# Kernel tuning notes

Hardware: AMD Instinct MI355X
Metric: run time of the kernel (lower is better)

## Reference

```python
import jax, jax.numpy as jnp
import numpy as np

INP = 256
OUP = 256
FGROUP = 16
CGROUP = 8
K = 3
STRIDE = 1
PAD = K // 2
B, H, W = 16, 64, 64
O1 = OUP * INP * K * K // CGROUP  # 73728, glgf output channels


def setup_inputs() -> dict:
    key = jax.random.key(0)
    ks = jax.random.split(key, 11)
    s = 0.1  # keep sigmoid pre-activations in a sane range
    return {
        "x": jax.random.normal(ks[0], (B, INP, H, W), jnp.float32),
        # GLGF generating the dynamic conv weights (oup*inp*k*k//cgroup outputs)
        "g1_fc1_l": jax.random.normal(ks[1], (INP, INP // FGROUP), jnp.float32) * s,
        "g1_fc1_g1": jax.random.normal(ks[2], (FGROUP, INP // FGROUP), jnp.float32) * s,
        "g1_fc1_g2": jax.random.normal(ks[3], (INP, FGROUP), jnp.float32) * s,
        "g1_fc2_l": jax.random.normal(ks[4], (O1,), jnp.float32) * s,
        "g1_fc2_g": jax.random.normal(ks[5], (INP,), jnp.float32) * s,
        # GLGF generating the per-channel output gate c (oup outputs)
        "g2_fc1_l": jax.random.normal(ks[6], (INP, INP // FGROUP), jnp.float32) * s,
        "g2_fc1_g1": jax.random.normal(ks[7], (FGROUP, INP // FGROUP), jnp.float32) * s,
        "g2_fc1_g2": jax.random.normal(ks[8], (INP, FGROUP), jnp.float32) * s,
        "g2_fc2_l": jax.random.normal(ks[9], (OUP,), jnp.float32) * s,
        "g2_fc2_g": jax.random.normal(ks[10], (INP,), jnp.float32) * s,
    }


def glgf(g, w1l, w1g1, w1g2, w2l, w2g):
    """GLGF applied to a [B, inp] gap vector (all convs are 1x1 -> grouped linears)."""
    b, inp = g.shape
    gp = inp // FGROUP
    gg = g.reshape(b, FGROUP, gp)
    # wn_fc1_l: grouped (fgroup) inp->inp; weight [inp, inp//fgroup]
    local = jnp.einsum('bgi,goi->bgo', gg, w1l.reshape(FGROUP, gp, gp)).reshape(b, inp)
    # wn_fc1_g2(wn_fc1_g1(x)): inp->fgroup (grouped) then fgroup->inp (dense)
    glob = jnp.einsum('bgi,gi->bg', gg, w1g1) @ w1g2.T  # [b, inp]
    h = jax.nn.sigmoid(local + glob)
    # wn_fc2_l: groups=inp, inp->O; weight [O] (1 input channel per output)
    O = w2l.shape[0]
    local2 = (h[:, :, None] * w2l.reshape(inp, O // inp)).reshape(b, O)
    # wn_fc2_g: dense inp->1, broadcast-added
    glob2 = h @ w2g  # [b]
    return local2 + glob2[:, None]


def reference(x, g1_fc1_l, g1_fc1_g1, g1_fc1_g2, g1_fc2_l, g1_fc2_g,
              g2_fc1_l, g2_fc1_g1, g2_fc1_g2, g2_fc2_l, g2_fc2_g):
    b = x.shape[0]
    gap = x.mean(axis=(2, 3))  # adaptive_avg_pool2d to 1x1 -> [b, inp]
    # generate per-sample grouped conv weights: [b, oup, inp//cgroup, k, k]
    xw = glgf(gap, g1_fc1_l, g1_fc1_g1, g1_fc1_g2, g1_fc2_l, g1_fc2_g)
    w = xw.reshape(b, OUP, INP // CGROUP, K, K)
    # torch's groups=b*cgroup batch-trick == per-sample conv with groups=cgroup
    def conv_one(xi, wi):
        return jax.lax.conv_general_dilated(
            xi[None], wi, (STRIDE, STRIDE), [(PAD, PAD), (PAD, PAD)],
            feature_group_count=CGROUP,
            dimension_numbers=('NCHW', 'OIHW', 'NCHW'))[0]
    y = jax.vmap(conv_one)(x, w)  # [b, oup, H, W]
    # per-sample, per-channel gate
    c = glgf(gap, g2_fc1_l, g2_fc1_g1, g2_fc1_g2, g2_fc2_l, g2_fc2_g)  # [b, oup]
    return y * c[:, :, None, None]
```

## Files before the change

kernel.cpp:

```cpp
#include <hip/hip_runtime.h>
#include <cstddef>
#include <cstdint>

typedef __attribute__((ext_vector_type(8))) short bf16x8;
typedef __attribute__((ext_vector_type(4))) unsigned short ushort4v;
typedef __attribute__((ext_vector_type(8))) unsigned short ushort8v;
typedef __attribute__((ext_vector_type(16))) float f32x16;

__device__ __forceinline__ unsigned short f2bf(float f) {
  union { float f; unsigned u; } v; v.f = f;
  unsigned r = v.u + 0x7FFFu + ((v.u >> 16) & 1u);
  return (unsigned short)(r >> 16);
}

__device__ __forceinline__ void gload16(const void* g, void* l) {
  __builtin_amdgcn_global_load_lds(
      (const __attribute__((address_space(1))) void*)(unsigned long long)(uintptr_t)g,
      (__attribute__((address_space(3))) void*)(unsigned)(uintptr_t)l, 16, 0, 0);
}

#define PADC 132
__global__ __launch_bounds__(256) void prep_kernel(
    const float* __restrict__ x, unsigned short* __restrict__ xt,
    float* __restrict__ partials) {
  __shared__ unsigned short cm[32 * PADC];
  __shared__ float sred[32][32];
  const int bid = blockIdx.x;
  const int wkr = ((bid & 7) << 9) | (bid >> 3);
  const int yp = wkr & 31, g = (wkr >> 5) & 7, b = wkr >> 8;
  const int y0 = yp * 2;
  const int tid = threadIdx.x;
  const float* xg = x + (size_t)(b * 256 + g * 32) * 4096;

  float csum[4];
#pragma unroll
  for (int j = 0; j < 4; ++j) {
    const int idx = tid + 256 * j;
    const int ic = idx >> 5;
    const int r = idx & 31;
    const int ry = r >> 4, gx4 = (r & 15) * 4;
    const float4 v = *reinterpret_cast<const float4*>(
        xg + (size_t)ic * 4096 + (y0 + ry) * 64 + gx4);
    csum[j] = v.x + v.y + v.z + v.w;
    ushort4v s;
    s[0] = f2bf(v.x); s[1] = f2bf(v.y); s[2] = f2bf(v.z); s[3] = f2bf(v.w);
    *reinterpret_cast<ushort4v*>(&cm[ic * PADC + ry * 64 + gx4]) = s;
  }
#pragma unroll
  for (int j = 0; j < 4; ++j) {
    const int ic = (tid >> 5) + 8 * j;
    sred[ic][tid & 31] = csum[j];
  }
  __syncthreads();

  if (tid < 32) {
    float s = 0.f;
#pragma unroll
    for (int i = 0; i < 32; ++i) s += sred[tid][i];
    partials[(size_t)(b * 256 + g * 32 + tid) * 32 + yp] = s;
  }

  const size_t xtb = (size_t)(b * 8 + g) * (66 * 66 * 32);
#pragma unroll
  for (int jj = 0; jj < 2; ++jj) {
    const int o = tid + 256 * jj;
    const int px = o >> 2, icq = o & 3;
    const int ry = px >> 6, gx = px & 63;
    ushort8v t;
#pragma unroll
    for (int c2 = 0; c2 < 8; ++c2) t[c2] = cm[(icq * 8 + c2) * PADC + px];
    *reinterpret_cast<ushort8v*>(
        &xt[xtb + ((size_t)(y0 + ry + 1) * 66 + (gx + 1)) * 32 + icq * 8]) = t;
  }

  const ushort8v z = {0, 0, 0, 0, 0, 0, 0, 0};
  if (tid < 16) {
    const int rr = tid >> 3;
    const int side = (tid >> 2) & 1;
    const int icq = tid & 3;
    const int col = side * 65;
    *reinterpret_cast<ushort8v*>(
        &xt[xtb + ((size_t)(y0 + rr + 1) * 66 + col) * 32 + icq * 8]) = z;
  }
  if (yp == 0 || yp == 31) {
    const int row = (yp == 0) ? 0 : 65;
    for (int o = tid; o < 66 * 4; o += 256) {
      const int col = o >> 2, icq = o & 3;
      *reinterpret_cast<ushort8v*>(
          &xt[xtb + ((size_t)row * 66 + col) * 32 + icq * 8]) = z;
    }
  }
}

__global__ __launch_bounds__(256) void glgf_pack(
    const float* __restrict__ partials,
    const float* __restrict__ w1l, const float* __restrict__ w1g1,
    const float* __restrict__ w1g2, const float* __restrict__ w2l,
    const float* __restrict__ w2g,
    const float* __restrict__ v1l, const float* __restrict__ v1g1,
    const float* __restrict__ v1g2, const float* __restrict__ v2l,
    const float* __restrict__ v2g,
    unsigned short* __restrict__ wpack) {
  __shared__ float gapL[256];
  __shared__ float t1L[16];
  __shared__ float h1L[256];
  __shared__ float red[256];
  __shared__ float cLs[32];
  const int bid = blockIdx.x;
  const int bg = ((bid & 7) << 4) | (bid >> 3);
  const int g = bg & 7, b = bg >> 3;
  const int c = threadIdx.x;
  {
    float s = 0.f;
    const float* pp = partials + (size_t)(b * 256 + c) * 32;
#pragma unroll
    for (int i = 0; i < 32; ++i) s += pp[i];
    gapL[c] = s * (1.f / 4096.f);
  }
  __syncthreads();

  const int gbase = c & ~15;
  float local1 = 0.f;
#pragma unroll
  for (int i = 0; i < 16; ++i) local1 += gapL[gbase + i] * w1l[c * 16 + i];
  if (c < 16) {
    float t = 0.f;
#pragma unroll
    for (int i = 0; i < 16; ++i) t += gapL[c * 16 + i] * w1g1[c * 16 + i];
    t1L[c] = t;
  }
  __syncthreads();
  float glob1 = 0.f;
#pragma unroll
  for (int gg = 0; gg < 16; ++gg) glob1 += t1L[gg] * w1g2[c * 16 + gg];
  const float h1 = 1.f / (1.f + expf(-(local1 + glob1)));
  h1L[c] = h1;
  red[c] = h1 * w2g[c];
  __syncthreads();
  for (int s = 128; s > 0; s >>= 1) {
    if (c < s) red[c] += red[c + s];
    __syncthreads();
  }
  const float glob2 = red[0];

  float local2 = 0.f;
#pragma unroll
  for (int i = 0; i < 16; ++i) local2 += gapL[gbase + i] * v1l[c * 16 + i];
  if (c < 16) {
    float t = 0.f;
#pragma unroll
    for (int i = 0; i < 16; ++i) t += gapL[c * 16 + i] * v1g1[c * 16 + i];
    t1L[c] = t;
  }
  __syncthreads();
  float glob1b = 0.f;
#pragma unroll
  for (int gg = 0; gg < 16; ++gg) glob1b += t1L[gg] * v1g2[c * 16 + gg];
  const float h2 = 1.f / (1.f + expf(-(local2 + glob1b)));
  red[c] = h2 * v2g[c];
  __syncthreads();
  for (int s = 128; s > 0; s >>= 1) {
    if (c < s) red[c] += red[c + s];
    __syncthreads();
  }
  if (c < 32) {
    const int o = g * 32 + c;
    float l = 0.f;
#pragma unroll
    for (int i = 0; i < 16; ++i) l += gapL[(o & ~15) + i] * v1l[o * 16 + i];
    float gl = 0.f;
#pragma unroll
    for (int gg = 0; gg < 16; ++gg) gl += t1L[gg] * v1g2[o * 16 + gg];
    const float h2o = 1.f / (1.f + expf(-(l + gl)));
    cLs[c] = h2o * v2l[o] + red[0];
  }
  __syncthreads();

  unsigned short* wpo = wpack + (size_t)bg * 9216;
#pragma unroll 4
  for (int it = 0; it < 36; ++it) {
    const int idx = it * 256 + c;
    const int kk = idx >> 9;
    const int rem = idx & 511;
    const int l = rem >> 3, e = rem & 7;
    const int oc = l & 31, hi = l >> 5;
    const int ic = ((kk & 1) << 4) + hi * 8 + e;
    const int sp = kk >> 1;
    const int o = (g << 5) + oc;
    const float wv = h1L[o] * w2l[o * 288 + ic * 9 + sp] + glob2;
    wpo[idx] = f2bf(wv * cLs[oc]);
  }
}

__global__ __launch_bounds__(256, 3) void conv_kernel(
    const unsigned short* __restrict__ wpack,
    const unsigned short* __restrict__ xt, float* __restrict__ out) {
  __shared__ __align__(16) unsigned short btile[2][8448];

  const int bid = blockIdx.x;
  const int wkr = ((bid & 7) << 7) | (bid >> 3);
  const int yq = wkr & 7;
  const int bg = wkr >> 3;
  const int g = bg & 7, b = bg >> 3;
  const int tid = threadIdx.x;
  const int lane = tid & 63, wave = tid >> 6;
  const int n = lane & 31, hi = lane >> 5;
  const int wr = wave >> 1, wc = wave & 1;

  const char* xbase = (const char*)xt + (size_t)bg * 278784;

  int s_boff[5];
#pragma unroll
  for (int i = 0; i < 5; ++i) {
    const int cc = (i * 256 + tid) < 1056 ? (i * 256 + tid) : 0;
    const int r = cc / 264, rem = cc % 264;
    const int cqs = rem / 66, px = rem % 66;
    const int cq = cqs ^ (px & 3);
    s_boff[i] = r * 4224 + px * 64 + cq * 16;
  }

  const unsigned short* wp = wpack + (size_t)bg * 9216 + lane * 8;
  bf16x8 a[18];
#pragma unroll
  for (int kk = 0; kk < 18; ++kk) {
    a[kk] = *reinterpret_cast<const bf16x8*>(wp + kk * 512);
    asm volatile("" : "+v"(a[kk]));
  }

  {
    const int yb = yq * 8 * 4224;
#pragma unroll
    for (int i = 0; i < 5; ++i)
      if (i * 256 + tid < 1056)
        gload16(xbase + yb + s_boff[i],
                (char*)&btile[0][0] + i * 4096 + wave * 1024);
  }
  asm volatile("s_waitcnt vmcnt(0) lgkmcnt(0)\n\ts_barrier" ::: "memory");
  __builtin_amdgcn_sched_barrier(0);

  float* ob0 = out + (size_t)(b * 256 + g * 32) * 4096 + wc * 32 + n +
               (size_t)(hi << 2) * 4096;

#pragma unroll
  for (int p = 0; p < 4; ++p) {
    const int side = p & 1;
    if (p < 3) {
      const int yb = (yq * 8 + (p + 1) * 2) * 4224;
#pragma unroll
      for (int i = 0; i < 5; ++i)
        if (i * 256 + tid < 1056)
          gload16(xbase + yb + s_boff[i],
                  (char*)&btile[side ^ 1][0] + i * 4096 + wave * 1024);
    }

    f32x16 acc;
#pragma unroll
    for (int i = 0; i < 16; ++i) acc[i] = 0.f;

    __builtin_amdgcn_s_setprio(1);
#pragma unroll
    for (int kk = 0; kk < 18; ++kk) {
      const int sp = kk >> 1;
      const int ky = sp / 3, kx = sp % 3;
      const int px2 = wc * 32 + n + kx;
      const int cq = ((kk & 1) << 1) + hi;
      const bf16x8 bf = *reinterpret_cast<const bf16x8*>(
          &btile[side][((((wr + ky) << 2) + (cq ^ (px2 & 3))) * 66 + px2) * 8]);
      acc = __builtin_amdgcn_mfma_f32_32x32x16_bf16(a[kk], bf, acc, 0, 0, 0);
    }
    __builtin_amdgcn_s_setprio(0);

    const int y = yq * 8 + p * 2 + wr;
    float* ob = ob0 + y * 64;
#pragma unroll
    for (int r = 0; r < 16; ++r) {
      const int row = (r & 3) + ((r >> 2) << 3);
      ob[(size_t)row * 4096] = acc[r];
    }

    if (p < 3) {
      asm volatile("s_waitcnt vmcnt(16) lgkmcnt(0)\n\ts_barrier" ::: "memory");
      __builtin_amdgcn_sched_barrier(0);
    }
  }
}

extern "C" void kernel_launch(void* const* d_in, const int* in_sizes, int n_in,
                              void* d_out, int out_size, void* d_ws,
                              size_t ws_size, hipStream_t stream) {
  const float* x    = (const float*)d_in[0];
  const float* w1l  = (const float*)d_in[1];
  const float* w1g1 = (const float*)d_in[2];
  const float* w1g2 = (const float*)d_in[3];
  const float* w2l  = (const float*)d_in[4];
  const float* w2g  = (const float*)d_in[5];
  const float* v1l  = (const float*)d_in[6];
  const float* v1g1 = (const float*)d_in[7];
  const float* v1g2 = (const float*)d_in[8];
  const float* v2l  = (const float*)d_in[9];
  const float* v2g  = (const float*)d_in[10];
  float* out = (float*)d_out;

  unsigned short* xt = (unsigned short*)d_ws;
  float* partials = (float*)(xt + 17842176);
  unsigned short* wpack = (unsigned short*)(partials + 131072);

  prep_kernel<<<4096, 256, 0, stream>>>(x, xt, partials);
  glgf_pack<<<128, 256, 0, stream>>>(partials, w1l, w1g1, w1g2, w2l, w2g,
                                     v1l, v1g1, v1g2, v2l, v2g, wpack);
  conv_kernel<<<1024, 256, 0, stream>>>(wpack, xt, out);
}
```

Measured before the change: 55.44 us.

## Split conv into one block per row pair, dropping double-buffer pipeline

The conv kernel now launches four times as many blocks, each computing a single pair of output rows with one LDS tile, instead of looping over four row pairs with a double-buffered prefetch. Weights are loaded from global memory inside the MFMA loop rather than held in 18 preloaded registers, which lowers register and LDS use so the launch bound can ask for 8 blocks per SIMD. The aim is to hide memory latency through occupancy instead of an explicit software pipeline. In exchange, the weight fragments are re-read by every block and the per-block load/compute overlap is lost.

```diff
diff --git a/kernel.cpp b/kernel.cpp
--- a/kernel.cpp
+++ b/kernel.cpp
@@ -192,15 +192,15 @@
   }
 }
 
-__global__ __launch_bounds__(256, 3) void conv_kernel(
+__global__ __launch_bounds__(256, 8) void conv_kernel(
     const unsigned short* __restrict__ wpack,
     const unsigned short* __restrict__ xt, float* __restrict__ out) {
-  __shared__ __align__(16) unsigned short btile[2][8448];
+  __shared__ __align__(16) unsigned short btile[8448];
 
   const int bid = blockIdx.x;
-  const int wkr = ((bid & 7) << 7) | (bid >> 3);
-  const int yq = wkr & 7;
-  const int bg = wkr >> 3;
+  const int wkr = ((bid & 7) << 9) | (bid >> 3);
+  const int yp = wkr & 31;
+  const int bg = wkr >> 5;
   const int g = bg & 7, b = bg >> 3;
   const int tid = threadIdx.x;
   const int lane = tid & 63, wave = tid >> 6;
@@ -208,80 +208,46 @@
   const int wr = wave >> 1, wc = wave & 1;
 
   const char* xbase = (const char*)xt + (size_t)bg * 278784;
-
-  int s_boff[5];
+  const int ys = yp * 2;
+
 #pragma unroll
   for (int i = 0; i < 5; ++i) {
-    const int cc = (i * 256 + tid) < 1056 ? (i * 256 + tid) : 0;
-    const int r = cc / 264, rem = cc % 264;
-    const int cqs = rem / 66, px = rem % 66;
-    const int cq = cqs ^ (px & 3);
-    s_boff[i] = r * 4224 + px * 64 + cq * 16;
-  }
-
-  const unsigned short* wp = wpack + (size_t)bg * 9216 + lane * 8;
-  bf16x8 a[18];
-#pragma unroll
-  for (int kk = 0; kk < 18; ++kk) {
-    a[kk] = *reinterpret_cast<const bf16x8*>(wp + kk * 512);
-    asm volatile("" : "+v"(a[kk]));
-  }
-
-  {
-    const int yb = yq * 8 * 4224;
-#pragma unroll
-    for (int i = 0; i < 5; ++i)
-      if (i * 256 + tid < 1056)
-        gload16(xbase + yb + s_boff[i],
-                (char*)&btile[0][0] + i * 4096 + wave * 1024);
+    const int li = i * 256 + tid;
+    if (li < 1056) {
+      const int r = li / 264, rem = li - r * 264;
+      const int cqs = rem / 66, px = rem % 66;
+      const int cq = cqs ^ (px & 3);
+      gload16(xbase + (ys + r) * 4224 + px * 64 + cq * 16,
+              (char*)btile + i * 4096 + wave * 1024);
+    }
   }
   asm volatile("s_waitcnt vmcnt(0) lgkmcnt(0)\n\ts_barrier" ::: "memory");
   __builtin_amdgcn_sched_barrier(0);
 
-  float* ob0 = out + (size_t)(b * 256 + g * 32) * 4096 + wc * 32 + n +
-               (size_t)(hi << 2) * 4096;
-
-#pragma unroll
-  for (int p = 0; p < 4; ++p) {
-    const int side = p & 1;
-    if (p < 3) {
-      const int yb = (yq * 8 + (p + 1) * 2) * 4224;
-#pragma unroll
-      for (int i = 0; i < 5; ++i)
-        if (i * 256 + tid < 1056)
-          gload16(xbase + yb + s_boff[i],
-                  (char*)&btile[side ^ 1][0] + i * 4096 + wave * 1024);
-    }
-
-    f32x16 acc;
-#pragma unroll
-    for (int i = 0; i < 16; ++i) acc[i] = 0.f;
-
-    __builtin_amdgcn_s_setprio(1);
-#pragma unroll
-    for (int kk = 0; kk < 18; ++kk) {
-      const int sp = kk >> 1;
-      const int ky = sp / 3, kx = sp % 3;
-      const int px2 = wc * 32 + n + kx;
-      const int cq = ((kk & 1) << 1) + hi;
-      const bf16x8 bf = *reinterpret_cast<const bf16x8*>(
-          &btile[side][((((wr + ky) << 2) + (cq ^ (px2 & 3))) * 66 + px2) * 8]);
-      acc = __builtin_amdgcn_mfma_f32_32x32x16_bf16(a[kk], bf, acc, 0, 0, 0);
-    }
-    __builtin_amdgcn_s_setprio(0);
-
-    const int y = yq * 8 + p * 2 + wr;
-    float* ob = ob0 + y * 64;
-#pragma unroll
-    for (int r = 0; r < 16; ++r) {
-      const int row = (r & 3) + ((r >> 2) << 3);
-      ob[(size_t)row * 4096] = acc[r];
-    }
-
-    if (p < 3) {
-      asm volatile("s_waitcnt vmcnt(16) lgkmcnt(0)\n\ts_barrier" ::: "memory");
-      __builtin_amdgcn_sched_barrier(0);
-    }
+  const unsigned short* wp = wpack + (size_t)bg * 9216 + lane * 8;
+  f32x16 acc;
+#pragma unroll
+  for (int i = 0; i < 16; ++i) acc[i] = 0.f;
+
+#pragma unroll
+  for (int kk = 0; kk < 18; ++kk) {
+    const int sp = kk >> 1;
+    const int ky = sp / 3, kx = sp % 3;
+    const int px2 = wc * 32 + n + kx;
+    const int cq = ((kk & 1) << 1) + hi;
+    const bf16x8 af = *reinterpret_cast<const bf16x8*>(wp + kk * 512);
+    const bf16x8 bf = *reinterpret_cast<const bf16x8*>(
+        &btile[((((wr + ky) << 2) + (cq ^ (px2 & 3))) * 66 + px2) * 8]);
+    acc = __builtin_amdgcn_mfma_f32_32x32x16_bf16(af, bf, acc, 0, 0, 0);
+  }
+
+  const int y = ys + wr;
+  float* ob = out + (size_t)(b * 256 + g * 32) * 4096 + y * 64 + wc * 32 + n +
+              (size_t)(hi << 2) * 4096;
+#pragma unroll
+  for (int r = 0; r < 16; ++r) {
+    const int row = (r & 3) + ((r >> 2) << 3);
+    ob[(size_t)row * 4096] = acc[r];
   }
 }
 
@@ -308,5 +274,5 @@
   prep_kernel<<<4096, 256, 0, stream>>>(x, xt, partials);
   glgf_pack<<<128, 256, 0, stream>>>(partials, w1l, w1g1, w1g2, w2l, w2g,
                                      v1l, v1g1, v1g2, v2l, v2g, wpack);
-  conv_kernel<<<1024, 256, 0, stream>>>(wpack, xt, out);
-}
+  conv_kernel<<<4096, 256, 0, stream>>>(wpack, xt, out);
+}
```

New measurement: 55.83 us. Within noise of the previous version (+0.7%).
